# Optimization experiments

Hardware: AMD Instinct MI355X
Metric: run time of the kernel (lower is better)

## Reference

```python
import jax, jax.numpy as jnp
import numpy as np

N, F, H = 1024, 512, 64
SPARSITY_WEIGHT = 0.01


def setup_inputs() -> dict:
    key = jax.random.key(0)
    ks = jax.random.split(key, 9)
    s = lambda fan_in: 1.0 / np.sqrt(fan_in)
    return {
        "node_features": jax.random.normal(ks[0], (N, F), dtype=jnp.float32),
        # node_transform: Linear(F->H), ReLU, Linear(H->H)
        "W1": jax.random.uniform(ks[1], (F, H), jnp.float32, -s(F), s(F)),
        "b1": jax.random.uniform(ks[2], (H,), jnp.float32, -s(F), s(F)),
        "W2": jax.random.uniform(ks[3], (H, H), jnp.float32, -s(H), s(H)),
        "b2": jax.random.uniform(ks[4], (H,), jnp.float32, -s(H), s(H)),
        # attn: Linear(2H->H), ReLU, Linear(H->1)
        "Wa1": jax.random.uniform(ks[5], (2 * H, H), jnp.float32, -s(2 * H), s(2 * H)),
        "ba1": jax.random.uniform(ks[6], (H,), jnp.float32, -s(2 * H), s(2 * H)),
        "wa2": jax.random.uniform(ks[7], (H,), jnp.float32, -s(H), s(H)),
        "ba2": jax.random.uniform(ks[8], (), jnp.float32, -s(H), s(H)),
        "temperature": jnp.float32(1.0),
    }


def reference(node_features, W1, b1, W2, b2, Wa1, ba1, wa2, ba2, temperature):
    # node transform: h = Linear(ReLU(Linear(x)))  -> [N, H]
    h = jax.nn.relu(node_features @ W1 + b1) @ W2 + b2
    # attn(concat(h_i, h_j)) decomposed GAT-style:
    # concat([h_i, h_j]) @ Wa1 == h_i @ Wa1[:H] + h_j @ Wa1[H:]
    e_i = h @ Wa1[:H]   # [N, H]
    e_j = h @ Wa1[H:]   # [N, H]
    z = jax.nn.relu(e_i[:, None, :] + e_j[None, :, :] + ba1)  # [N, N, H]
    scores = jnp.einsum("ijh,h->ij", z, wa2) + ba2            # [N, N]
    scores = scores / jnp.clip(temperature, 0.1, 5.0)
    scores = (scores + scores.T) * 0.5
    adjacency = jax.nn.sigmoid(scores)
    sparsity_loss = SPARSITY_WEIGHT * jnp.mean(jnp.abs(adjacency))
    return (adjacency, sparsity_loss)
```

## Files before the change

### kernel.cpp

```cpp
#include <hip/hip_runtime.h>
#include <cmath>

#define NN 1024
#define FF 512
#define HH 64
#define NPAIRS 528

__global__ __launch_bounds__(1024, 4) void k1_transform(
    const float* __restrict__ x, const float* __restrict__ W1,
    const float* __restrict__ b1, const float* __restrict__ W2,
    const float* __restrict__ b2, const float* __restrict__ Wa1,
    const float* __restrict__ ba1,
    float* __restrict__ ei, float* __restrict__ ejb)
{
    __shared__ float xs[4][516];
    __shared__ float ts[4][68];
    __shared__ float hs[4][68];
    __shared__ float pp[16][4][68];
    const int tid = threadIdx.x;
    const int row0 = blockIdx.x * 4;

    if (tid < 512) {
        int r = tid >> 7;
        int cc = (tid & 127) << 2;
        *reinterpret_cast<float4*>(&xs[r][cc]) =
            *reinterpret_cast<const float4*>(x + (row0 + r) * FF + cc);
    }
    __syncthreads();

    const int ks = tid >> 6;
    const int r  = (tid >> 4) & 3;
    const int cg = (tid & 15) << 2;

    {
        float4 acc = make_float4(0.f, 0.f, 0.f, 0.f);
        const int k0 = ks * 32;
        #pragma unroll 4
        for (int k = k0; k < k0 + 32; k += 4) {
            float4 a  = *reinterpret_cast<const float4*>(&xs[r][k]);
            float4 w0 = *reinterpret_cast<const float4*>(W1 + (k + 0) * HH + cg);
            float4 w1 = *reinterpret_cast<const float4*>(W1 + (k + 1) * HH + cg);
            float4 w2 = *reinterpret_cast<const float4*>(W1 + (k + 2) * HH + cg);
            float4 w3 = *reinterpret_cast<const float4*>(W1 + (k + 3) * HH + cg);
            acc.x += a.x * w0.x + a.y * w1.x + a.z * w2.x + a.w * w3.x;
            acc.y += a.x * w0.y + a.y * w1.y + a.z * w2.y + a.w * w3.y;
            acc.z += a.x * w0.z + a.y * w1.z + a.z * w2.z + a.w * w3.z;
            acc.w += a.x * w0.w + a.y * w1.w + a.z * w2.w + a.w * w3.w;
        }
        *reinterpret_cast<float4*>(&pp[ks][r][cg]) = acc;
    }
    __syncthreads();
    if (ks == 0) {
        float4 s0 = *reinterpret_cast<const float4*>(&pp[0][r][cg]);
        #pragma unroll
        for (int q = 1; q < 16; ++q) {
            float4 p = *reinterpret_cast<const float4*>(&pp[q][r][cg]);
            s0.x += p.x; s0.y += p.y; s0.z += p.z; s0.w += p.w;
        }
        float4 bv = *reinterpret_cast<const float4*>(b1 + cg);
        float4 t;
        t.x = fmaxf(s0.x + bv.x, 0.f);
        t.y = fmaxf(s0.y + bv.y, 0.f);
        t.z = fmaxf(s0.z + bv.z, 0.f);
        t.w = fmaxf(s0.w + bv.w, 0.f);
        *reinterpret_cast<float4*>(&ts[r][cg]) = t;
    }
    __syncthreads();

    {
        float4 acc = make_float4(0.f, 0.f, 0.f, 0.f);
        const int k = ks * 4;
        float4 a  = *reinterpret_cast<const float4*>(&ts[r][k]);
        float4 w0 = *reinterpret_cast<const float4*>(W2 + (k + 0) * HH + cg);
        float4 w1 = *reinterpret_cast<const float4*>(W2 + (k + 1) * HH + cg);
        float4 w2 = *reinterpret_cast<const float4*>(W2 + (k + 2) * HH + cg);
        float4 w3 = *reinterpret_cast<const float4*>(W2 + (k + 3) * HH + cg);
        acc.x += a.x * w0.x + a.y * w1.x + a.z * w2.x + a.w * w3.x;
        acc.y += a.x * w0.y + a.y * w1.y + a.z * w2.y + a.w * w3.y;
        acc.z += a.x * w0.z + a.y * w1.z + a.z * w2.z + a.w * w3.z;
        acc.w += a.x * w0.w + a.y * w1.w + a.z * w2.w + a.w * w3.w;
        *reinterpret_cast<float4*>(&pp[ks][r][cg]) = acc;
    }
    __syncthreads();
    if (ks == 0) {
        float4 s0 = *reinterpret_cast<const float4*>(&pp[0][r][cg]);
        #pragma unroll
        for (int q = 1; q < 16; ++q) {
            float4 p = *reinterpret_cast<const float4*>(&pp[q][r][cg]);
            s0.x += p.x; s0.y += p.y; s0.z += p.z; s0.w += p.w;
        }
        float4 bv = *reinterpret_cast<const float4*>(b2 + cg);
        float4 h;
        h.x = s0.x + bv.x; h.y = s0.y + bv.y;
        h.z = s0.z + bv.z; h.w = s0.w + bv.w;
        *reinterpret_cast<float4*>(&hs[r][cg]) = h;
    }
    __syncthreads();

    {
        const float* Wb = Wa1 + (ks >> 3) * HH * HH;
        float4 acc = make_float4(0.f, 0.f, 0.f, 0.f);
        const int k0 = (ks & 7) * 8;
        #pragma unroll
        for (int k = k0; k < k0 + 8; k += 4) {
            float4 a  = *reinterpret_cast<const float4*>(&hs[r][k]);
            float4 w0 = *reinterpret_cast<const float4*>(Wb + (k + 0) * HH + cg);
            float4 w1 = *reinterpret_cast<const float4*>(Wb + (k + 1) * HH + cg);
            float4 w2 = *reinterpret_cast<const float4*>(Wb + (k + 2) * HH + cg);
            float4 w3 = *reinterpret_cast<const float4*>(Wb + (k + 3) * HH + cg);
            acc.x += a.x * w0.x + a.y * w1.x + a.z * w2.x + a.w * w3.x;
            acc.y += a.x * w0.y + a.y * w1.y + a.z * w2.y + a.w * w3.y;
            acc.z += a.x * w0.z + a.y * w1.z + a.z * w2.z + a.w * w3.z;
            acc.w += a.x * w0.w + a.y * w1.w + a.z * w2.w + a.w * w3.w;
        }
        *reinterpret_cast<float4*>(&pp[ks][r][cg]) = acc;
    }
    __syncthreads();
    if (ks == 0) {
        float4 s0 = *reinterpret_cast<const float4*>(&pp[0][r][cg]);
        #pragma unroll
        for (int q = 1; q < 8; ++q) {
            float4 p = *reinterpret_cast<const float4*>(&pp[q][r][cg]);
            s0.x += p.x; s0.y += p.y; s0.z += p.z; s0.w += p.w;
        }
        *reinterpret_cast<float4*>(ei + (row0 + r) * HH + cg) = s0;
    } else if (ks == 8) {
        float4 s0 = *reinterpret_cast<const float4*>(&pp[8][r][cg]);
        #pragma unroll
        for (int q = 9; q < 16; ++q) {
            float4 p = *reinterpret_cast<const float4*>(&pp[q][r][cg]);
            s0.x += p.x; s0.y += p.y; s0.z += p.z; s0.w += p.w;
        }
        float4 bv = *reinterpret_cast<const float4*>(ba1 + cg);
        s0.x += bv.x; s0.y += bv.y; s0.z += bv.z; s0.w += bv.w;
        *reinterpret_cast<float4*>(ejb + (row0 + r) * HH + cg) = s0;
    }
}

__global__ __launch_bounds__(256, 4) void k2_pair(
    const float* __restrict__ ei, const float* __restrict__ ejb,
    const float* __restrict__ wa2, const float* __restrict__ ba2,
    const float* __restrict__ temp,
    float* __restrict__ out, float* __restrict__ partials)
{
    __shared__ float stg[4][32][68];
    __shared__ float T[32][33];
    __shared__ float wl[64];
    __shared__ float wsum[4];
    const int tid = threadIdx.x;

    int I = 0, rem = blockIdx.x, rl = 32;
    while (rem >= rl) { rem -= rl; ++I; --rl; }
    const int J = I + rem;
    const int iBase = I * 32, jBase = J * 32;
    const bool off = (I != J);

    {
        const int rr = tid >> 4;
        const int cq = (tid & 15) << 2;
        const float* s0 = ei  + iBase * HH;
        const float* s1 = ei  + jBase * HH;
        const float* s2 = ejb + iBase * HH;
        const float* s3 = ejb + jBase * HH;
        #pragma unroll
        for (int l = 0; l < 2; ++l) {
            int r = rr + 16 * l;
            *reinterpret_cast<float4*>(&stg[0][r][cq]) =
                *reinterpret_cast<const float4*>(s0 + r * HH + cq);
            *reinterpret_cast<float4*>(&stg[1][r][cq]) =
                *reinterpret_cast<const float4*>(s1 + r * HH + cq);
            *reinterpret_cast<float4*>(&stg[2][r][cq]) =
                *reinterpret_cast<const float4*>(s2 + r * HH + cq);
            *reinterpret_cast<float4*>(&stg[3][r][cq]) =
                *reinterpret_cast<const float4*>(s3 + r * HH + cq);
        }
    }
    if (tid < 16) {
        *reinterpret_cast<float4*>(&wl[tid * 4]) =
            *reinterpret_cast<const float4*>(wa2 + tid * 4);
    }
    __syncthreads();

    const int c  = tid & 31;
    const int r0 = tid >> 5;

    float d1[4] = {0.f, 0.f, 0.f, 0.f};
    float d2[4] = {0.f, 0.f, 0.f, 0.f};

    #pragma unroll 4
    for (int h = 0; h < HH; h += 4) {
        float4 w  = *reinterpret_cast<const float4*>(&wl[h]);
        {
            float4 Bj = *reinterpret_cast<const float4*>(&stg[3][c][h]);
            #pragma unroll
            for (int m = 0; m < 4; ++m) {
                float4 Ai = *reinterpret_cast<const float4*>(&stg[0][r0 + 8 * m][h]);
                d1[m] += fmaxf(Ai.x + Bj.x, 0.f) * w.x
                       + fmaxf(Ai.y + Bj.y, 0.f) * w.y
                       + fmaxf(Ai.z + Bj.z, 0.f) * w.z
                       + fmaxf(Ai.w + Bj.w, 0.f) * w.w;
            }
        }
        {
            float4 Ej = *reinterpret_cast<const float4*>(&stg[1][c][h]);
            #pragma unroll
            for (int m = 0; m < 4; ++m) {
                float4 Bi = *reinterpret_cast<const float4*>(&stg[2][r0 + 8 * m][h]);
                d2[m] += fmaxf(Ej.x + Bi.x, 0.f) * w.x
                       + fmaxf(Ej.y + Bi.y, 0.f) * w.y
                       + fmaxf(Ej.z + Bi.z, 0.f) * w.z
                       + fmaxf(Ej.w + Bi.w, 0.f) * w.w;
            }
        }
    }

    const float t = fminf(fmaxf(temp[0], 0.1f), 5.0f);
    const float invt = 1.0f / t;
    const float bb = ba2[0];

    float adj4[4];
    float lsum = 0.f;
    #pragma unroll
    for (int m = 0; m < 4; ++m) {
        const int row = r0 + 8 * m;
        float v = (0.5f * (d1[m] + d2[m]) + bb) * invt;
        float adj = 1.0f / (1.0f + __expf(-v));
        adj4[m] = adj;
        out[(iBase + row) * NN + jBase + c] = adj;
        lsum += adj;
    }

    if (off) {
        #pragma unroll
        for (int m = 0; m < 4; ++m) T[c][r0 + 8 * m] = adj4[m];
        __syncthreads();
        #pragma unroll
        for (int m = 0; m < 4; ++m) {
            const int rr = r0 + 8 * m;
            out[(jBase + rr) * NN + iBase + c] = T[rr][c];
        }
        lsum *= 2.0f;
    }

    float w = lsum;
    #pragma unroll
    for (int o = 32; o > 0; o >>= 1) w += __shfl_down(w, o);
    if ((tid & 63) == 0) wsum[tid >> 6] = w;
    __syncthreads();
    if (tid == 0) {
        partials[blockIdx.x] = (wsum[0] + wsum[1]) + (wsum[2] + wsum[3]);
    }
}

__global__ __launch_bounds__(256) void k3_reduce(
    const float* __restrict__ partials, float* __restrict__ out_loss)
{
    __shared__ float wsum[4];
    const int tid = threadIdx.x;
    float v = partials[tid] + partials[tid + 256];
    if (tid < 16) v += partials[tid + 512];
    #pragma unroll
    for (int o = 32; o > 0; o >>= 1) v += __shfl_down(v, o);
    if ((tid & 63) == 0) wsum[tid >> 6] = v;
    __syncthreads();
    if (tid == 0) {
        float tot = (wsum[0] + wsum[1]) + (wsum[2] + wsum[3]);
        *out_loss = 0.01f * tot / (float)(NN * NN);
    }
}

extern "C" void kernel_launch(void* const* d_in, const int* in_sizes, int n_in,
                              void* d_out, int out_size, void* d_ws, size_t ws_size,
                              hipStream_t stream)
{
    const float* x    = (const float*)d_in[0];
    const float* W1   = (const float*)d_in[1];
    const float* b1   = (const float*)d_in[2];
    const float* W2   = (const float*)d_in[3];
    const float* b2   = (const float*)d_in[4];
    const float* Wa1  = (const float*)d_in[5];
    const float* ba1  = (const float*)d_in[6];
    const float* wa2  = (const float*)d_in[7];
    const float* ba2  = (const float*)d_in[8];
    const float* temp = (const float*)d_in[9];
    float* out = (float*)d_out;

    float* ei    = (float*)d_ws;
    float* ejb   = ei + NN * HH;
    float* parts = ejb + NN * HH;

    k1_transform<<<NN / 4, 1024, 0, stream>>>(x, W1, b1, W2, b2, Wa1, ba1, ei, ejb);
    k2_pair<<<NPAIRS, 256, 0, stream>>>(ei, ejb, wa2, ba2, temp, out, parts);
    k3_reduce<<<1, 256, 0, stream>>>(parts, out + NN * NN);
}
```

Measured before the change: 27.85 us.

## Compute raw pair scores once, then symmetrize and apply sigmoid in a separate pass

Result: no change. 27.37 us (-1.7%).

```diff
diff --git a/kernel.cpp b/kernel.cpp
--- a/kernel.cpp
+++ b/kernel.cpp
@@ -137,108 +137,128 @@
     }
 }
 
-__global__ __launch_bounds__(256, 4) void k2_pair(
+__global__ __launch_bounds__(512, 2) void k2_raw(
     const float* __restrict__ ei, const float* __restrict__ ejb,
-    const float* __restrict__ wa2, const float* __restrict__ ba2,
-    const float* __restrict__ temp,
-    float* __restrict__ out, float* __restrict__ partials)
-{
-    __shared__ float stg[4][32][68];
-    __shared__ float T[32][33];
+    const float* __restrict__ wa2, float* __restrict__ sraw)
+{
+    __shared__ float eil[64][68];
+    __shared__ float ejl[64][68];
     __shared__ float wl[64];
+    const int tid = threadIdx.x;
+    const int i0 = (blockIdx.x >> 4) * 64;
+    const int j0 = (blockIdx.x & 15) * 64;
+
+    {
+        const int rr = tid >> 4;
+        const int cq = (tid & 15) << 2;
+        #pragma unroll
+        for (int l = 0; l < 2; ++l) {
+            int r = rr + 32 * l;
+            *reinterpret_cast<float4*>(&eil[r][cq]) =
+                *reinterpret_cast<const float4*>(ei + (i0 + r) * HH + cq);
+            *reinterpret_cast<float4*>(&ejl[r][cq]) =
+                *reinterpret_cast<const float4*>(ejb + (j0 + r) * HH + cq);
+        }
+    }
+    if (tid < 16) {
+        *reinterpret_cast<float4*>(&wl[tid * 4]) =
+            *reinterpret_cast<const float4*>(wa2 + tid * 4);
+    }
+    __syncthreads();
+
+    const int ty = tid >> 5;
+    const int tx = tid & 31;
+    float acc[4][2] = {};
+
+    #pragma unroll 4
+    for (int h = 0; h < HH; h += 4) {
+        float4 w  = *reinterpret_cast<const float4*>(&wl[h]);
+        float4 B0 = *reinterpret_cast<const float4*>(&ejl[tx][h]);
+        float4 B1 = *reinterpret_cast<const float4*>(&ejl[tx + 32][h]);
+        #pragma unroll
+        for (int m = 0; m < 4; ++m) {
+            float4 A = *reinterpret_cast<const float4*>(&eil[ty + 16 * m][h]);
+            acc[m][0] += fmaxf(A.x + B0.x, 0.f) * w.x
+                       + fmaxf(A.y + B0.y, 0.f) * w.y
+                       + fmaxf(A.z + B0.z, 0.f) * w.z
+                       + fmaxf(A.w + B0.w, 0.f) * w.w;
+            acc[m][1] += fmaxf(A.x + B1.x, 0.f) * w.x
+                       + fmaxf(A.y + B1.y, 0.f) * w.y
+                       + fmaxf(A.z + B1.z, 0.f) * w.z
+                       + fmaxf(A.w + B1.w, 0.f) * w.w;
+        }
+    }
+    #pragma unroll
+    for (int m = 0; m < 4; ++m) {
+        const int row = i0 + ty + 16 * m;
+        sraw[row * NN + j0 + tx]      = acc[m][0];
+        sraw[row * NN + j0 + tx + 32] = acc[m][1];
+    }
+}
+
+__global__ __launch_bounds__(256, 4) void k3_sym(
+    float* __restrict__ s, const float* __restrict__ ba2,
+    const float* __restrict__ temp, float* __restrict__ partials)
+{
+    __shared__ float A[32][36];
+    __shared__ float Bt[32][33];
     __shared__ float wsum[4];
     const int tid = threadIdx.x;
 
     int I = 0, rem = blockIdx.x, rl = 32;
     while (rem >= rl) { rem -= rl; ++I; --rl; }
     const int J = I + rem;
-    const int iBase = I * 32, jBase = J * 32;
+    const int bi = I * 32, bj = J * 32;
     const bool off = (I != J);
 
-    {
-        const int rr = tid >> 4;
-        const int cq = (tid & 15) << 2;
-        const float* s0 = ei  + iBase * HH;
-        const float* s1 = ei  + jBase * HH;
-        const float* s2 = ejb + iBase * HH;
-        const float* s3 = ejb + jBase * HH;
-        #pragma unroll
-        for (int l = 0; l < 2; ++l) {
-            int r = rr + 16 * l;
-            *reinterpret_cast<float4*>(&stg[0][r][cq]) =
-                *reinterpret_cast<const float4*>(s0 + r * HH + cq);
-            *reinterpret_cast<float4*>(&stg[1][r][cq]) =
-                *reinterpret_cast<const float4*>(s1 + r * HH + cq);
-            *reinterpret_cast<float4*>(&stg[2][r][cq]) =
-                *reinterpret_cast<const float4*>(s2 + r * HH + cq);
-            *reinterpret_cast<float4*>(&stg[3][r][cq]) =
-                *reinterpret_cast<const float4*>(s3 + r * HH + cq);
-        }
-    }
-    if (tid < 16) {
-        *reinterpret_cast<float4*>(&wl[tid * 4]) =
-            *reinterpret_cast<const float4*>(wa2 + tid * 4);
-    }
-    __syncthreads();
-
-    const int c  = tid & 31;
-    const int r0 = tid >> 5;
-
-    float d1[4] = {0.f, 0.f, 0.f, 0.f};
-    float d2[4] = {0.f, 0.f, 0.f, 0.f};
-
-    #pragma unroll 4
-    for (int h = 0; h < HH; h += 4) {
-        float4 w  = *reinterpret_cast<const float4*>(&wl[h]);
-        {
-            float4 Bj = *reinterpret_cast<const float4*>(&stg[3][c][h]);
-            #pragma unroll
-            for (int m = 0; m < 4; ++m) {
-                float4 Ai = *reinterpret_cast<const float4*>(&stg[0][r0 + 8 * m][h]);
-                d1[m] += fmaxf(Ai.x + Bj.x, 0.f) * w.x
-                       + fmaxf(Ai.y + Bj.y, 0.f) * w.y
-                       + fmaxf(Ai.z + Bj.z, 0.f) * w.z
-                       + fmaxf(Ai.w + Bj.w, 0.f) * w.w;
-            }
-        }
-        {
-            float4 Ej = *reinterpret_cast<const float4*>(&stg[1][c][h]);
-            #pragma unroll
-            for (int m = 0; m < 4; ++m) {
-                float4 Bi = *reinterpret_cast<const float4*>(&stg[2][r0 + 8 * m][h]);
-                d2[m] += fmaxf(Ej.x + Bi.x, 0.f) * w.x
-                       + fmaxf(Ej.y + Bi.y, 0.f) * w.y
-                       + fmaxf(Ej.z + Bi.z, 0.f) * w.z
-                       + fmaxf(Ej.w + Bi.w, 0.f) * w.w;
-            }
-        }
-    }
+    const int rb = tid >> 3;
+    const int cb = (tid & 7) << 2;
+
+    {
+        *reinterpret_cast<float4*>(&A[rb][cb]) =
+            *reinterpret_cast<const float4*>(s + (bi + rb) * NN + bj + cb);
+        float4 bv = *reinterpret_cast<const float4*>(s + (bj + rb) * NN + bi + cb);
+        Bt[cb + 0][rb] = bv.x;
+        Bt[cb + 1][rb] = bv.y;
+        Bt[cb + 2][rb] = bv.z;
+        Bt[cb + 3][rb] = bv.w;
+    }
+    __syncthreads();
 
     const float t = fminf(fmaxf(temp[0], 0.1f), 5.0f);
     const float invt = 1.0f / t;
     const float bb = ba2[0];
 
-    float adj4[4];
+    float vals[4];
     float lsum = 0.f;
     #pragma unroll
-    for (int m = 0; m < 4; ++m) {
-        const int row = r0 + 8 * m;
-        float v = (0.5f * (d1[m] + d2[m]) + bb) * invt;
+    for (int e = 0; e < 4; ++e) {
+        const int c = cb + e;
+        float v = (0.5f * (A[rb][c] + Bt[rb][c]) + bb) * invt;
         float adj = 1.0f / (1.0f + __expf(-v));
-        adj4[m] = adj;
-        out[(iBase + row) * NN + jBase + c] = adj;
+        vals[e] = adj;
         lsum += adj;
     }
+    __syncthreads();
+
+    {
+        float4 o;
+        o.x = vals[0]; o.y = vals[1]; o.z = vals[2]; o.w = vals[3];
+        *reinterpret_cast<float4*>(s + (bi + rb) * NN + bj + cb) = o;
+        A[rb][cb + 0] = vals[0];
+        A[rb][cb + 1] = vals[1];
+        A[rb][cb + 2] = vals[2];
+        A[rb][cb + 3] = vals[3];
+    }
 
     if (off) {
-        #pragma unroll
-        for (int m = 0; m < 4; ++m) T[c][r0 + 8 * m] = adj4[m];
         __syncthreads();
-        #pragma unroll
-        for (int m = 0; m < 4; ++m) {
-            const int rr = r0 + 8 * m;
-            out[(jBase + rr) * NN + iBase + c] = T[rr][c];
-        }
+        float4 o;
+        o.x = A[cb + 0][rb];
+        o.y = A[cb + 1][rb];
+        o.z = A[cb + 2][rb];
+        o.w = A[cb + 3][rb];
+        *reinterpret_cast<float4*>(s + (bj + rb) * NN + bi + cb) = o;
         lsum *= 2.0f;
     }
 
@@ -252,7 +272,7 @@
     }
 }
 
-__global__ __launch_bounds__(256) void k3_reduce(
+__global__ __launch_bounds__(256) void k4_reduce(
     const float* __restrict__ partials, float* __restrict__ out_loss)
 {
     __shared__ float wsum[4];
@@ -290,6 +310,7 @@
     float* parts = ejb + NN * HH;
 
     k1_transform<<<NN / 4, 1024, 0, stream>>>(x, W1, b1, W2, b2, Wa1, ba1, ei, ejb);
-    k2_pair<<<NPAIRS, 256, 0, stream>>>(ei, ejb, wa2, ba2, temp, out, parts);
-    k3_reduce<<<1, 256, 0, stream>>>(parts, out + NN * NN);
-}
+    k2_raw<<<256, 512, 0, stream>>>(ei, ejb, wa2, out);
+    k3_sym<<<NPAIRS, 256, 0, stream>>>(out, ba2, temp, parts);
+    k4_reduce<<<1, 256, 0, stream>>>(parts, out + NN * NN);
+}
```
